# Optimization experiments

Measured on AMD Instinct MI355X. Metric: run time of the kernel, lower is better.

Reference implementation:

```python
import jax, jax.numpy as jnp
import numpy as np

N_USERS, N_ITEMS, EMB_DIM, N_INTENTS, N_EDGES, N_LAYERS = 50000, 100000, 64, 128, 3000000, 2
N_NODES = N_USERS + N_ITEMS


def _l2norm(x, eps=1e-8):
    # F.normalize(p=2, dim=-1, eps): x / max(||x||, eps)
    n = jnp.sqrt(jnp.sum(x * x, axis=-1, keepdims=True))
    return x / jnp.maximum(n, eps)


def setup_inputs() -> dict:
    key = jax.random.key(0)
    k0, k1, k2, k3, k4, k5 = jax.random.split(key, 6)
    xav_e = np.sqrt(2.0 / (N_NODES + EMB_DIM)).astype(np.float32)
    xav_i = np.sqrt(2.0 / (EMB_DIM + N_INTENTS)).astype(np.float32)
    return {
        "user_emb": jax.random.normal(k0, (N_USERS, EMB_DIM), jnp.float32) * xav_e,
        "item_emb": jax.random.normal(k1, (N_ITEMS, EMB_DIM), jnp.float32) * xav_e,
        "user_intent": jax.random.normal(k2, (EMB_DIM, N_INTENTS), jnp.float32) * xav_i,
        "item_intent": jax.random.normal(k3, (EMB_DIM, N_INTENTS), jnp.float32) * xav_i,
        "all_h": jax.random.randint(k4, (N_EDGES,), 0, N_NODES, jnp.int32),
        "all_t": jax.random.randint(k5, (N_EDGES,), 0, N_NODES, jnp.int32),
    }


def reference(user_emb, item_emb, user_intent, item_intent, all_h, all_t):
    E = all_h.shape[0]

    def spmm(vals, x):
        # y[h] += vals * x[t]  over edges  (torch_sparse.spmm)
        return jax.ops.segment_sum(vals[:, None] * x[all_t], all_h, num_segments=N_NODES)

    # _cal_sparse_adj: G = D^-1/2 A D^-1/2 on the unweighted edge list
    deg = jax.ops.segment_sum(jnp.ones((E,), jnp.float32), all_h, num_segments=N_NODES)
    d_inv_sqrt = jnp.where(deg > 0, deg, 1.0) ** -0.5 * (deg > 0)
    g_values = d_inv_sqrt[all_h] * d_inv_sqrt[all_t]

    def adaptive_values(src):
        # _adaptive_mask: cosine-sim edge weights, row-normalized
        he = _l2norm(src[all_h])
        te = _l2norm(src[all_t])
        edge_alpha = (jnp.sum(he * te, axis=1) + 1.0) * 0.5  # in [0,1]
        row_sum = jax.ops.segment_sum(edge_alpha, all_h, num_segments=N_NODES)
        d_inv = jnp.where(row_sum > 0, 1.0 / jnp.where(row_sum > 0, row_sum, 1.0), 0.0)
        return d_inv[all_h] * edge_alpha

    emb = jnp.concatenate([user_emb, item_emb], axis=0)  # [N, d]
    acc = emb
    for _ in range(N_LAYERS):
        gnn = spmm(g_values, emb)
        u, it = emb[:N_USERS], emb[N_USERS:]
        u_int = jax.nn.softmax(u @ user_intent, axis=1) @ user_intent.T
        i_int = jax.nn.softmax(it @ item_intent, axis=1) @ item_intent.T
        int_e = jnp.concatenate([u_int, i_int], axis=0)
        gaa = spmm(adaptive_values(gnn), emb)
        iaa = spmm(adaptive_values(int_e), emb)
        emb = gnn + int_e + gaa + iaa + emb
        acc = acc + emb
    # torch: sum over stacked layer embeddings == initial + each layer output
    return acc
```

## Files before the change

kernel.cpp:

```cpp
#include <hip/hip_runtime.h>
#include <hip/hip_bf16.h>

#define N_USERS   50000
#define N_ITEMS   100000
#define N_NODES   150000
#define DIM       64
#define N_INTENTS 128
#define N_EDGES   3000000
#define PSHIFT    9
#define PROWS     (1 << PSHIFT)
#define NPART     ((N_NODES + PROWS - 1) >> PSHIFT)
#define CHUNK     16384
#define NCHB      ((N_EDGES + CHUNK - 1) / CHUNK)

typedef __attribute__((ext_vector_type(8))) short short8v;
typedef __attribute__((ext_vector_type(4))) float f32x4;

static __device__ __forceinline__ float wsum64(float v){
#pragma unroll
  for (int m = 32; m >= 1; m >>= 1) v += __shfl_xor(v, m, 64);
  return v;
}
static __device__ __forceinline__ float wmax64(float v){
#pragma unroll
  for (int m = 32; m >= 1; m >>= 1) v = fmaxf(v, __shfl_xor(v, m, 64));
  return v;
}

template<int CTRL>
static __device__ __forceinline__ float dpp_ror_add(float x){
  int t = __builtin_amdgcn_update_dpp(0, __builtin_bit_cast(int, x),
                                      CTRL, 0xF, 0xF, true);
  return x + __builtin_bit_cast(float, t);
}
static __device__ __forceinline__ float row16_allsum(float x){
  x = dpp_ror_add<0x128>(x);
  x = dpp_ror_add<0x124>(x);
  x = dpp_ror_add<0x122>(x);
  x = dpp_ror_add<0x121>(x);
  return x;
}
template<int CTRL>
static __device__ __forceinline__ float dpp_ror_max(float x){
  int t = __builtin_amdgcn_update_dpp(0, __builtin_bit_cast(int, x),
                                      CTRL, 0xF, 0xF, true);
  return fmaxf(x, __builtin_bit_cast(float, t));
}
static __device__ __forceinline__ float row16_allmax(float x){
  x = dpp_ror_max<0x128>(x);
  x = dpp_ror_max<0x124>(x);
  x = dpp_ror_max<0x122>(x);
  x = dpp_ror_max<0x121>(x);
  return x;
}

static __device__ __forceinline__ unsigned short f2bf(float x){
  __hip_bfloat16 h = __float2bfloat16(x);
  return __builtin_bit_cast(unsigned short, h);
}
static __device__ __forceinline__ float bf_lo(unsigned int v){
  return __builtin_bit_cast(float, v << 16);
}
static __device__ __forceinline__ float bf_hi(unsigned int v){
  return __builtin_bit_cast(float, v & 0xFFFF0000u);
}
static __device__ __forceinline__ float bfval(unsigned short h){
  return __builtin_bit_cast(float, (unsigned int)h << 16);
}
static __device__ __forceinline__ void split2(float x, unsigned short& hi,
                                              unsigned short& lo){
  hi = f2bf(x);
  lo = f2bf(x - bfval(hi));
}

__global__ void k_init(const float* __restrict__ ue, const float* __restrict__ ie,
                       float* __restrict__ emb, float* __restrict__ acc,
                       unsigned short* __restrict__ embb){
  int i = blockIdx.x * 256 + threadIdx.x;
  if (i >= N_NODES * DIM) return;
  float v = (i < N_USERS * DIM) ? ue[i] : ie[i - N_USERS * DIM];
  emb[i] = v; acc[i] = v; embb[i] = f2bf(v);
}

__global__ void k_deg(const int* __restrict__ h, int* __restrict__ deg){
  int e = blockIdx.x * 256 + threadIdx.x;
  if (e < N_EDGES) atomicAdd(&deg[h[e]], 1);
}

__global__ void k_scan1(const int* __restrict__ deg, int* __restrict__ tmp,
                        int* __restrict__ aux){
  __shared__ int s[256];
  int t = threadIdx.x, i = blockIdx.x * 256 + t;
  int v = (i < N_NODES) ? deg[i] : 0;
  s[t] = v; __syncthreads();
  for (int off = 1; off < 256; off <<= 1){
    int x = (t >= off) ? s[t - off] : 0;
    __syncthreads();
    s[t] += x;
    __syncthreads();
  }
  if (i < N_NODES) tmp[i] = s[t];
  if (t == 255) aux[blockIdx.x] = s[255];
}

__global__ __launch_bounds__(1024) void k_scan2(int* __restrict__ aux, int n){
  __shared__ int s[1024];
  int t = threadIdx.x;
  int v = (t < n) ? aux[t] : 0;
  s[t] = v; __syncthreads();
  for (int off = 1; off < 1024; off <<= 1){
    int x = (t >= off) ? s[t - off] : 0;
    __syncthreads();
    s[t] += x;
    __syncthreads();
  }
  if (t < n) aux[t] = s[t] - v;
}

__global__ void k_rowptr(const int* __restrict__ tmp, const int* __restrict__ deg,
                         const int* __restrict__ aux, int* __restrict__ rp,
                         float* __restrict__ dis, int* __restrict__ gcur){
  int i = blockIdx.x * 256 + threadIdx.x;
  if (i < N_NODES){
    int v = aux[i >> 8] + tmp[i] - deg[i];
    rp[i] = v;
    int d = deg[i];
    dis[i] = (d > 0) ? (1.f / sqrtf((float)d)) : 0.f;
    if ((i & (PROWS - 1)) == 0) gcur[i >> PSHIFT] = v;
  }
  if (i == 0) rp[N_NODES] = N_EDGES;
}

__global__ __launch_bounds__(256) void k_part1(const int* __restrict__ h,
                                               const int* __restrict__ t,
                                               int* __restrict__ gcur,
                                               unsigned int* __restrict__ stg){
  __shared__ int hist[NPART];
  __shared__ int base[NPART];
  __shared__ int cnt2[NPART];
  int tid = threadIdx.x;
  int s = blockIdx.x * CHUNK;
  int e = min(s + CHUNK, N_EDGES);
  for (int p = tid; p < NPART; p += 256){ hist[p] = 0; cnt2[p] = 0; }
  __syncthreads();
  for (int i = s + tid; i < e; i += 256)
    atomicAdd(&hist[h[i] >> PSHIFT], 1);
  __syncthreads();
  for (int p = tid; p < NPART; p += 256){
    int c = hist[p];
    base[p] = c ? atomicAdd(&gcur[p], c) : 0;
  }
  __syncthreads();
  for (int i = s + tid; i < e; i += 256){
    int hh = h[i];
    int part = hh >> PSHIFT;
    int pos = base[part] + atomicAdd(&cnt2[part], 1);
    stg[pos] = ((unsigned)t[i] << PSHIFT) | (unsigned)(hh & (PROWS - 1));
  }
}

__global__ __launch_bounds__(256) void k_part2(const int* __restrict__ rp,
                                               const unsigned int* __restrict__ stg,
                                               int* __restrict__ t_csr){
  __shared__ int cur[PROWS];
  int b = blockIdx.x, tid = threadIdx.x;
  int row0 = b << PSHIFT;
  int rows = min(PROWS, N_NODES - row0);
  for (int i = tid; i < rows; i += 256) cur[i] = rp[row0 + i];
  __syncthreads();
  int s = rp[row0], e = rp[row0 + rows];
  for (int i = s + tid; i < e; i += 256){
    unsigned int v = stg[i];
    int pos = atomicAdd(&cur[v & (PROWS - 1)], 1);
    t_csr[pos] = (int)(v >> PSHIFT);
  }
}

__global__ void k_spmm_gnn(const int* __restrict__ rp, const int* __restrict__ t_csr,
                           const float* __restrict__ dis,
                           const unsigned short* __restrict__ embb,
                           float* __restrict__ gnn, unsigned short* __restrict__ hgA){
  int w = (blockIdx.x * 256 + threadIdx.x) >> 6;
  int lane = threadIdx.x & 63;
  if (w >= N_NODES) return;
  int slot = lane >> 3, sub = lane & 7;
  int s = rp[w], e = rp[w + 1];
  float a0=0.f,a1=0.f,a2=0.f,a3=0.f,a4=0.f,a5=0.f,a6=0.f,a7=0.f;
  for (int i = s + slot; i < e; i += 8){
    int t = t_csr[i];
    float wt = dis[t];
    uint4 ev = *(const uint4*)(embb + (size_t)t * 64 + 8 * sub);
    a0 = fmaf(wt, bf_lo(ev.x), a0); a1 = fmaf(wt, bf_hi(ev.x), a1);
    a2 = fmaf(wt, bf_lo(ev.y), a2); a3 = fmaf(wt, bf_hi(ev.y), a3);
    a4 = fmaf(wt, bf_lo(ev.z), a4); a5 = fmaf(wt, bf_hi(ev.z), a5);
    a6 = fmaf(wt, bf_lo(ev.w), a6); a7 = fmaf(wt, bf_hi(ev.w), a7);
  }
#pragma unroll
  for (int m = 8; m <= 32; m <<= 1){
    a0 += __shfl_xor(a0, m, 64); a1 += __shfl_xor(a1, m, 64);
    a2 += __shfl_xor(a2, m, 64); a3 += __shfl_xor(a3, m, 64);
    a4 += __shfl_xor(a4, m, 64); a5 += __shfl_xor(a5, m, 64);
    a6 += __shfl_xor(a6, m, 64); a7 += __shfl_xor(a7, m, 64);
  }
  float dw = dis[w];
  float g0 = dw*a0, g1 = dw*a1, g2 = dw*a2, g3 = dw*a3;
  float g4 = dw*a4, g5 = dw*a5, g6 = dw*a6, g7 = dw*a7;
  float sq = g0*g0 + g1*g1 + g2*g2 + g3*g3 + g4*g4 + g5*g5 + g6*g6 + g7*g7;
#pragma unroll
  for (int m = 1; m <= 4; m <<= 1) sq += __shfl_xor(sq, m, 64);
  float invn = 1.f / fmaxf(sqrtf(sq), 1e-8f);
  if (slot == 0){
    float4 v0 = make_float4(g0, g1, g2, g3);
    float4 v1 = make_float4(g4, g5, g6, g7);
    ((float4*)gnn)[w * 16 + 2 * sub]     = v0;
    ((float4*)gnn)[w * 16 + 2 * sub + 1] = v1;
    uint4 ob;
    ob.x = (unsigned)f2bf(g0*invn) | ((unsigned)f2bf(g1*invn) << 16);
    ob.y = (unsigned)f2bf(g2*invn) | ((unsigned)f2bf(g3*invn) << 16);
    ob.z = (unsigned)f2bf(g4*invn) | ((unsigned)f2bf(g5*invn) << 16);
    ob.w = (unsigned)f2bf(g6*invn) | ((unsigned)f2bf(g7*invn) << 16);
    *(uint4*)(hgA + (size_t)w * 64 + 8 * sub) = ob;
  }
}

__global__ void k_wprep(const float* __restrict__ wu, const float* __restrict__ wi,
                        unsigned short* __restrict__ wbuf){
  const float* W = blockIdx.x ? wi : wu;
  unsigned short* seg = wbuf + blockIdx.x * 32768;
  int tid = threadIdx.x;
  for (int i = tid; i < DIM * N_INTENTS; i += 256){
    unsigned short h, l; split2(W[i], h, l);
    seg[16384 + i] = h; seg[24576 + i] = l;
  }
  for (int idx = tid; idx < 16 * 64; idx += 256){
    int f = idx >> 6, lane = idx & 63;
    int nt = f >> 1, ks = f & 1, g = lane >> 4, c = lane & 15;
    int in = 16 * nt + c;
#pragma unroll
    for (int e = 0; e < 8; e++){
      int d = 8 * g + e + 32 * ks;
      unsigned short h, l; split2(W[d * N_INTENTS + in], h, l);
      seg[f * 512 + lane * 8 + e] = h;
      seg[8192 + f * 512 + lane * 8 + e] = l;
    }
  }
}

__global__ __launch_bounds__(256) void k_intent_mfma(
    const unsigned short* __restrict__ wseg, const float* __restrict__ emb,
    unsigned short* __restrict__ out_bf, unsigned short* __restrict__ hgB,
    int base_node, int count){
  __shared__ __align__(16) unsigned int Pl[4][2048];
  int wid = threadIdx.x >> 6, lane = threadIdx.x & 63;
  int tile = blockIdx.x * 4 + wid;
  if (tile * 16 >= count) return;
  int g = lane >> 4, c = lane & 15;

  const float4* erow = (const float4*)(emb + (size_t)(base_node + tile * 16 + c) * DIM);
  float4 ea0 = erow[2 * g],     eb0 = erow[2 * g + 1];
  float4 ea1 = erow[8 + 2 * g], eb1 = erow[9 + 2 * g];
  short8v ehi[2], elo[2];
  {
    float xs[16] = {ea0.x, ea0.y, ea0.z, ea0.w, eb0.x, eb0.y, eb0.z, eb0.w,
                    ea1.x, ea1.y, ea1.z, ea1.w, eb1.x, eb1.y, eb1.z, eb1.w};
#pragma unroll
    for (int ksi = 0; ksi < 2; ksi++)
#pragma unroll
      for (int e = 0; e < 8; e++){
        unsigned short h, l; split2(xs[ksi * 8 + e], h, l);
        ehi[ksi][e] = (short)h; elo[ksi][e] = (short)l;
      }
  }

  const uint4* w1hi = (const uint4*)wseg;
  const uint4* w1lo = (const uint4*)(wseg + 8192);
  f32x4 acc1[8];
#pragma unroll
  for (int nt = 0; nt < 8; nt++){
    f32x4 a = {0.f, 0.f, 0.f, 0.f};
#pragma unroll
    for (int ks = 0; ks < 2; ks++){
      short8v wh = __builtin_bit_cast(short8v, w1hi[(nt * 2 + ks) * 64 + lane]);
      short8v wl = __builtin_bit_cast(short8v, w1lo[(nt * 2 + ks) * 64 + lane]);
      a = __builtin_amdgcn_mfma_f32_16x16x32_bf16(ehi[ks], wh, a, 0, 0, 0);
      a = __builtin_amdgcn_mfma_f32_16x16x32_bf16(elo[ks], wh, a, 0, 0, 0);
      a = __builtin_amdgcn_mfma_f32_16x16x32_bf16(ehi[ks], wl, a, 0, 0, 0);
    }
    acc1[nt] = a;
  }

  unsigned int* pw = &Pl[wid][0];
#pragma unroll
  for (int r = 0; r < 4; r++){
    float m = acc1[0][r];
#pragma unroll
    for (int nt = 1; nt < 8; nt++) m = fmaxf(m, acc1[nt][r]);
    m = row16_allmax(m);
    float p[8];
    float s = 0.f;
#pragma unroll
    for (int nt = 0; nt < 8; nt++){ p[nt] = __expf(acc1[nt][r] - m); s += p[nt]; }
    s = row16_allsum(s);
    float inv = 1.f / s;
    int node = 4 * g + r;
    int swz = (node & 7) << 2;
    int base = node * 128 + c;
#pragma unroll
    for (int nt = 0; nt < 8; nt++){
      float v = p[nt] * inv;
      unsigned short h, l; split2(v, h, l);
      pw[(base + 16 * nt) ^ swz] = (unsigned int)h | ((unsigned int)l << 16);
    }
  }

  const uint4* pr = (const uint4*)pw;
  short8v phf[4], plf[4];
  int sw = (c & 7) << 2;
#pragma unroll
  for (int ks = 0; ks < 4; ks++){
    int i0 = c * 128 + 8 * g + 32 * ks;
    uint4 ra = pr[(i0 ^ sw) >> 2];
    uint4 rb = pr[((i0 + 4) ^ sw) >> 2];
    unsigned int q[8] = {ra.x, ra.y, ra.z, ra.w, rb.x, rb.y, rb.z, rb.w};
#pragma unroll
    for (int e = 0; e < 8; e++){
      phf[ks][e] = (short)(q[e] & 0xFFFFu);
      plf[ks][e] = (short)(q[e] >> 16);
    }
  }

  const uint4* w2hi = (const uint4*)(wseg + 16384);
  const uint4* w2lo = (const uint4*)(wseg + 24576);
  f32x4 acc2[4];
#pragma unroll
  for (int nt = 0; nt < 4; nt++){
    f32x4 a = {0.f, 0.f, 0.f, 0.f};
#pragma unroll
    for (int ks = 0; ks < 4; ks++){
      int fi = (16 * nt + c) * 16 + ks * 4 + g;
      short8v wh = __builtin_bit_cast(short8v, w2hi[fi]);
      short8v wl = __builtin_bit_cast(short8v, w2lo[fi]);
      a = __builtin_amdgcn_mfma_f32_16x16x32_bf16(phf[ks], wh, a, 0, 0, 0);
      a = __builtin_amdgcn_mfma_f32_16x16x32_bf16(plf[ks], wh, a, 0, 0, 0);
      a = __builtin_amdgcn_mfma_f32_16x16x32_bf16(phf[ks], wl, a, 0, 0, 0);
    }
    acc2[nt] = a;
  }

#pragma unroll
  for (int r = 0; r < 4; r++){
    float sq = 0.f;
#pragma unroll
    for (int nt = 0; nt < 4; nt++) sq = fmaf(acc2[nt][r], acc2[nt][r], sq);
    sq = row16_allsum(sq);
    float invn = 1.f / fmaxf(sqrtf(sq), 1e-8f);
    size_t gbase = (size_t)(base_node + tile * 16 + 4 * g + r) * DIM + c;
#pragma unroll
    for (int nt = 0; nt < 4; nt++){
      float v = acc2[nt][r];
      out_bf[gbase + 16 * nt] = f2bf(v);
      hgB[gbase + 16 * nt] = f2bf(v * invn);
    }
  }
}

__global__ void k_adafuse(const int* __restrict__ rp, const int* __restrict__ t_csr,
                          const unsigned short* __restrict__ hgA,
                          const unsigned short* __restrict__ hgB,
                          const uint2* __restrict__ inte_bf2,
                          const unsigned short* __restrict__ embb,
                          const float* __restrict__ emb,
                          float* __restrict__ gnn_io, float* __restrict__ acc,
                          uint2* __restrict__ embb_next2){
  int w = (blockIdx.x * 256 + threadIdx.x) >> 6;
  int lane = threadIdx.x & 63;
  if (w >= N_NODES) return;
  int g = lane >> 4, c = lane & 15;
  const unsigned short* wa = hgA + (size_t)w * 64;
  const unsigned short* wb = hgB + (size_t)w * 64;
  short8v bA0 = *(const short8v*)(wa + 8 * g);
  short8v bA1 = *(const short8v*)(wa + 8 * g + 32);
  short8v bB0 = *(const short8v*)(wb + 8 * g);
  short8v bB1 = *(const short8v*)(wb + 8 * g + 32);
  int s = rp[w], e = rp[w + 1];
  float4 s1 = make_float4(0.f, 0.f, 0.f, 0.f);
  float4 s2 = make_float4(0.f, 0.f, 0.f, 0.f);
  float r1 = 0.f, r2 = 0.f;
  for (int i = s; i < e; i += 16){
    int ia = i + c; if (ia >= e) ia = e - 1;
    int t = t_csr[ia];
    const unsigned short* ra = hgA + (size_t)t * 64;
    const unsigned short* rb = hgB + (size_t)t * 64;
    short8v aA0 = *(const short8v*)(ra + 8 * g);
    short8v aA1 = *(const short8v*)(ra + 8 * g + 32);
    short8v aB0 = *(const short8v*)(rb + 8 * g);
    short8v aB1 = *(const short8v*)(rb + 8 * g + 32);
    f32x4 p = {0.f, 0.f, 0.f, 0.f};
    f32x4 q = {0.f, 0.f, 0.f, 0.f};
    p = __builtin_amdgcn_mfma_f32_16x16x32_bf16(aA0, bA0, p, 0, 0, 0);
    p = __builtin_amdgcn_mfma_f32_16x16x32_bf16(aA1, bA1, p, 0, 0, 0);
    q = __builtin_amdgcn_mfma_f32_16x16x32_bf16(aB0, bB0, q, 0, 0, 0);
    q = __builtin_amdgcn_mfma_f32_16x16x32_bf16(aB1, bB1, q, 0, 0, 0);
#pragma unroll
    for (int r = 0; r < 4; r++){
      int ei = i + 4 * g + r;
      bool valid = ei < e;
      float a1v = valid ? fmaf(p[r], 0.5f, 0.5f) : 0.f;
      float a2v = valid ? fmaf(q[r], 0.5f, 0.5f) : 0.f;
      r1 += a1v; r2 += a2v;
      int tt = t_csr[valid ? ei : (e - 1)];
      uint2 ev = *(const uint2*)(embb + (size_t)tt * 64 + 4 * c);
      float v0 = bf_lo(ev.x), v1 = bf_hi(ev.x), v2 = bf_lo(ev.y), v3 = bf_hi(ev.y);
      s1.x = fmaf(a1v, v0, s1.x); s1.y = fmaf(a1v, v1, s1.y);
      s1.z = fmaf(a1v, v2, s1.z); s1.w = fmaf(a1v, v3, s1.w);
      s2.x = fmaf(a2v, v0, s2.x); s2.y = fmaf(a2v, v1, s2.y);
      s2.z = fmaf(a2v, v2, s2.z); s2.w = fmaf(a2v, v3, s2.w);
    }
  }
#pragma unroll
  for (int m = 16; m <= 32; m <<= 1){
    s1.x += __shfl_xor(s1.x, m, 64); s1.y += __shfl_xor(s1.y, m, 64);
    s1.z += __shfl_xor(s1.z, m, 64); s1.w += __shfl_xor(s1.w, m, 64);
    s2.x += __shfl_xor(s2.x, m, 64); s2.y += __shfl_xor(s2.y, m, 64);
    s2.z += __shfl_xor(s2.z, m, 64); s2.w += __shfl_xor(s2.w, m, 64);
    r1   += __shfl_xor(r1,   m, 64); r2   += __shfl_xor(r2,   m, 64);
  }
  float d1 = (r1 > 0.f) ? 1.f / r1 : 0.f;
  float d2 = (r2 > 0.f) ? 1.f / r2 : 0.f;
  if (g == 0){
    int idx4 = w * 16 + c;
    float4 gg = ((float4*)gnn_io)[idx4];
    uint2 it = inte_bf2[idx4];
    float4 em = ((const float4*)emb)[idx4];
    float4 nv;
    nv.x = gg.x + bf_lo(it.x) + em.x + d1 * s1.x + d2 * s2.x;
    nv.y = gg.y + bf_hi(it.x) + em.y + d1 * s1.y + d2 * s2.y;
    nv.z = gg.z + bf_lo(it.y) + em.z + d1 * s1.z + d2 * s2.z;
    nv.w = gg.w + bf_hi(it.y) + em.w + d1 * s1.w + d2 * s2.w;
    ((float4*)gnn_io)[idx4] = nv;
    float4 ac = ((float4*)acc)[idx4];
    ac.x += nv.x; ac.y += nv.y; ac.z += nv.z; ac.w += nv.w;
    ((float4*)acc)[idx4] = ac;
    uint2 ob;
    ob.x = (unsigned)f2bf(nv.x) | ((unsigned)f2bf(nv.y) << 16);
    ob.y = (unsigned)f2bf(nv.z) | ((unsigned)f2bf(nv.w) << 16);
    embb_next2[idx4] = ob;
  }
}

extern "C" void kernel_launch(void* const* d_in, const int* in_sizes, int n_in,
                              void* d_out, int out_size, void* d_ws, size_t ws_size,
                              hipStream_t stream){
  const float* ue = (const float*)d_in[0];
  const float* ie = (const float*)d_in[1];
  const float* wu = (const float*)d_in[2];
  const float* wi = (const float*)d_in[3];
  const int* all_h = (const int*)d_in[4];
  const int* all_t = (const int*)d_in[5];
  float* acc = (float*)d_out;

  char* p = (char*)d_ws;
  auto take = [&](size_t bytes)->char*{
    char* r = p; p += (bytes + 255) & ~size_t(255); return r;
  };
  float*  embA  = (float*)take(sizeof(float) * N_NODES * DIM);
  float*  embB  = (float*)take(sizeof(float) * N_NODES * DIM);
  unsigned short* hgA = (unsigned short*)take(sizeof(short) * N_NODES * DIM);
  unsigned short* hgB = (unsigned short*)take(sizeof(short) * N_NODES * DIM);
  unsigned short* inte_bf = (unsigned short*)take(sizeof(short) * N_NODES * DIM);
  unsigned short* embbA   = (unsigned short*)take(sizeof(short) * N_NODES * DIM);
  unsigned short* embbB   = (unsigned short*)take(sizeof(short) * N_NODES * DIM);
  unsigned short* wbuf    = (unsigned short*)take(sizeof(short) * 2 * 32768);
  int*    t_csr = (int*)take(sizeof(int) * N_EDGES);
  float*  dis   = (float*)take(sizeof(float) * N_NODES);
  int*    deg   = (int*)take(sizeof(int) * N_NODES);
  int*    tmp   = (int*)take(sizeof(int) * N_NODES);
  int*    aux   = (int*)take(sizeof(int) * 1024);
  int*    rp    = (int*)take(sizeof(int) * (N_NODES + 1));
  int*    gcur  = (int*)take(sizeof(int) * NPART);
  if ((size_t)(p - (char*)d_ws) > ws_size) return;
  unsigned int* stg = (unsigned int*)hgA;

  const int ELEM_B  = (N_NODES * DIM + 255) / 256;
  const int NODEW_B = (N_NODES * 64 + 255) / 256;
  const int EDGE_B  = (N_EDGES + 255) / 256;
  const int NODE_B  = (N_NODES + 255) / 256;

  hipMemsetAsync(deg, 0, sizeof(int) * N_NODES, stream);
  k_init<<<ELEM_B, 256, 0, stream>>>(ue, ie, embA, acc, embbA);
  k_wprep<<<2, 256, 0, stream>>>(wu, wi, wbuf);
  k_deg<<<EDGE_B, 256, 0, stream>>>(all_h, deg);
  k_scan1<<<NODE_B, 256, 0, stream>>>(deg, tmp, aux);
  k_scan2<<<1, 1024, 0, stream>>>(aux, NODE_B);
  k_rowptr<<<NODE_B, 256, 0, stream>>>(tmp, deg, aux, rp, dis, gcur);
  k_part1<<<NCHB, 256, 0, stream>>>(all_h, all_t, gcur, stg);
  k_part2<<<NPART, 256, 0, stream>>>(rp, stg, t_csr);

  const int UT_B = ((N_USERS / 16) + 3) / 4;
  const int IT_B = ((N_ITEMS / 16) + 3) / 4;

  float* eA = embA;
  float* eB = embB;
  unsigned short* ebA = embbA;
  unsigned short* ebB = embbB;
  for (int layer = 0; layer < 2; layer++){
    k_spmm_gnn<<<NODEW_B, 256, 0, stream>>>(rp, t_csr, dis, ebA, eB, hgA);
    k_intent_mfma<<<UT_B, 256, 0, stream>>>(wbuf, eA, inte_bf, hgB, 0, N_USERS);
    k_intent_mfma<<<IT_B, 256, 0, stream>>>(wbuf + 32768, eA, inte_bf, hgB,
                                            N_USERS, N_ITEMS);
    k_adafuse<<<NODEW_B, 256, 0, stream>>>(rp, t_csr, hgA, hgB,
                                           (const uint2*)inte_bf, ebA,
                                           eA, eB, acc, (uint2*)ebB);
    float* t = eA; eA = eB; eB = t;
    unsigned short* tb = ebA; ebA = ebB; ebB = tb;
  }
}
```

Baseline: 1.018 ms.

## Interleave normalized feature buffers per node and software-pipeline gathers in SpMM kernels

Merges the two normalized bf16 feature arrays into one interleaved 128-wide row per node, so each adaptive-weight gather reads one contiguous 256-byte row instead of two separate 128-byte rows. Both the gnn SpMM and the adaptive fused kernel now prefetch the next iteration's neighbor indices and embedding loads before consuming the current ones, hiding gather latency. The cost is more live registers, which may reduce occupancy, plus clamped redundant loads at row ends.

New measurement: 1.024 ms. Within noise of the previous version (+0.6%).

```diff
diff --git a/kernel.cpp b/kernel.cpp
--- a/kernel.cpp
+++ b/kernel.cpp
@@ -179,21 +179,29 @@
 __global__ void k_spmm_gnn(const int* __restrict__ rp, const int* __restrict__ t_csr,
                            const float* __restrict__ dis,
                            const unsigned short* __restrict__ embb,
-                           float* __restrict__ gnn, unsigned short* __restrict__ hgA){
+                           float* __restrict__ gnn, unsigned short* __restrict__ hgAB){
   int w = (blockIdx.x * 256 + threadIdx.x) >> 6;
   int lane = threadIdx.x & 63;
   if (w >= N_NODES) return;
   int slot = lane >> 3, sub = lane & 7;
   int s = rp[w], e = rp[w + 1];
   float a0=0.f,a1=0.f,a2=0.f,a3=0.f,a4=0.f,a5=0.f,a6=0.f,a7=0.f;
-  for (int i = s + slot; i < e; i += 8){
-    int t = t_csr[i];
-    float wt = dis[t];
-    uint4 ev = *(const uint4*)(embb + (size_t)t * 64 + 8 * sub);
-    a0 = fmaf(wt, bf_lo(ev.x), a0); a1 = fmaf(wt, bf_hi(ev.x), a1);
-    a2 = fmaf(wt, bf_lo(ev.y), a2); a3 = fmaf(wt, bf_hi(ev.y), a3);
-    a4 = fmaf(wt, bf_lo(ev.z), a4); a5 = fmaf(wt, bf_hi(ev.z), a5);
-    a6 = fmaf(wt, bf_lo(ev.w), a6); a7 = fmaf(wt, bf_hi(ev.w), a7);
+  if (e > s){
+    int i = s + slot;
+    int t0 = t_csr[min(i, e - 1)];
+    int t1 = t_csr[min(i + 8, e - 1)];
+    float wt0 = dis[t0];
+    uint4 ev0 = *(const uint4*)(embb + (size_t)t0 * 64 + 8 * sub);
+    for (; i < e; i += 8){
+      int t2 = t_csr[min(i + 16, e - 1)];
+      float wt1 = dis[t1];
+      uint4 ev1 = *(const uint4*)(embb + (size_t)t1 * 64 + 8 * sub);
+      a0 = fmaf(wt0, bf_lo(ev0.x), a0); a1 = fmaf(wt0, bf_hi(ev0.x), a1);
+      a2 = fmaf(wt0, bf_lo(ev0.y), a2); a3 = fmaf(wt0, bf_hi(ev0.y), a3);
+      a4 = fmaf(wt0, bf_lo(ev0.z), a4); a5 = fmaf(wt0, bf_hi(ev0.z), a5);
+      a6 = fmaf(wt0, bf_lo(ev0.w), a6); a7 = fmaf(wt0, bf_hi(ev0.w), a7);
+      wt0 = wt1; ev0 = ev1; t1 = t2;
+    }
   }
 #pragma unroll
   for (int m = 8; m <= 32; m <<= 1){
@@ -219,7 +227,7 @@
     ob.y = (unsigned)f2bf(g2*invn) | ((unsigned)f2bf(g3*invn) << 16);
     ob.z = (unsigned)f2bf(g4*invn) | ((unsigned)f2bf(g5*invn) << 16);
     ob.w = (unsigned)f2bf(g6*invn) | ((unsigned)f2bf(g7*invn) << 16);
-    *(uint4*)(hgA + (size_t)w * 64 + 8 * sub) = ob;
+    *(uint4*)(hgAB + (size_t)w * 128 + 8 * sub) = ob;
   }
 }
 
@@ -248,7 +256,7 @@
 
 __global__ __launch_bounds__(256) void k_intent_mfma(
     const unsigned short* __restrict__ wseg, const float* __restrict__ emb,
-    unsigned short* __restrict__ out_bf, unsigned short* __restrict__ hgB,
+    unsigned short* __restrict__ out_bf, unsigned short* __restrict__ hgAB,
     int base_node, int count){
   __shared__ __align__(16) unsigned int Pl[4][2048];
   int wid = threadIdx.x >> 6, lane = threadIdx.x & 63;
@@ -354,19 +362,20 @@
     for (int nt = 0; nt < 4; nt++) sq = fmaf(acc2[nt][r], acc2[nt][r], sq);
     sq = row16_allsum(sq);
     float invn = 1.f / fmaxf(sqrtf(sq), 1e-8f);
-    size_t gbase = (size_t)(base_node + tile * 16 + 4 * g + r) * DIM + c;
+    size_t node = (size_t)(base_node + tile * 16 + 4 * g + r);
+    unsigned short* hw = hgAB + node * 128 + 64;
+    size_t obase = node * DIM + c;
 #pragma unroll
     for (int nt = 0; nt < 4; nt++){
       float v = acc2[nt][r];
-      out_bf[gbase + 16 * nt] = f2bf(v);
-      hgB[gbase + 16 * nt] = f2bf(v * invn);
+      out_bf[obase + 16 * nt] = f2bf(v);
+      hw[16 * nt + c] = f2bf(v * invn);
     }
   }
 }
 
 __global__ void k_adafuse(const int* __restrict__ rp, const int* __restrict__ t_csr,
-                          const unsigned short* __restrict__ hgA,
-                          const unsigned short* __restrict__ hgB,
+                          const unsigned short* __restrict__ hgAB,
                           const uint2* __restrict__ inte_bf2,
                           const unsigned short* __restrict__ embb,
                           const float* __restrict__ emb,
@@ -376,45 +385,95 @@
   int lane = threadIdx.x & 63;
   if (w >= N_NODES) return;
   int g = lane >> 4, c = lane & 15;
-  const unsigned short* wa = hgA + (size_t)w * 64;
-  const unsigned short* wb = hgB + (size_t)w * 64;
-  short8v bA0 = *(const short8v*)(wa + 8 * g);
-  short8v bA1 = *(const short8v*)(wa + 8 * g + 32);
-  short8v bB0 = *(const short8v*)(wb + 8 * g);
-  short8v bB1 = *(const short8v*)(wb + 8 * g + 32);
+  const unsigned short* wr = hgAB + (size_t)w * 128;
+  short8v bA0 = *(const short8v*)(wr + 8 * g);
+  short8v bA1 = *(const short8v*)(wr + 8 * g + 32);
+  short8v bB0 = *(const short8v*)(wr + 64 + 8 * g);
+  short8v bB1 = *(const short8v*)(wr + 96 + 8 * g);
   int s = rp[w], e = rp[w + 1];
   float4 s1 = make_float4(0.f, 0.f, 0.f, 0.f);
   float4 s2 = make_float4(0.f, 0.f, 0.f, 0.f);
   float r1 = 0.f, r2 = 0.f;
-  for (int i = s; i < e; i += 16){
-    int ia = i + c; if (ia >= e) ia = e - 1;
+  if (e > s){
+    int ia = min(s + c, e - 1);
     int t = t_csr[ia];
-    const unsigned short* ra = hgA + (size_t)t * 64;
-    const unsigned short* rb = hgB + (size_t)t * 64;
+    const unsigned short* ra = hgAB + (size_t)t * 128;
     short8v aA0 = *(const short8v*)(ra + 8 * g);
     short8v aA1 = *(const short8v*)(ra + 8 * g + 32);
-    short8v aB0 = *(const short8v*)(rb + 8 * g);
-    short8v aB1 = *(const short8v*)(rb + 8 * g + 32);
-    f32x4 p = {0.f, 0.f, 0.f, 0.f};
-    f32x4 q = {0.f, 0.f, 0.f, 0.f};
-    p = __builtin_amdgcn_mfma_f32_16x16x32_bf16(aA0, bA0, p, 0, 0, 0);
-    p = __builtin_amdgcn_mfma_f32_16x16x32_bf16(aA1, bA1, p, 0, 0, 0);
-    q = __builtin_amdgcn_mfma_f32_16x16x32_bf16(aB0, bB0, q, 0, 0, 0);
-    q = __builtin_amdgcn_mfma_f32_16x16x32_bf16(aB1, bB1, q, 0, 0, 0);
-#pragma unroll
-    for (int r = 0; r < 4; r++){
-      int ei = i + 4 * g + r;
-      bool valid = ei < e;
-      float a1v = valid ? fmaf(p[r], 0.5f, 0.5f) : 0.f;
-      float a2v = valid ? fmaf(q[r], 0.5f, 0.5f) : 0.f;
-      r1 += a1v; r2 += a2v;
-      int tt = t_csr[valid ? ei : (e - 1)];
-      uint2 ev = *(const uint2*)(embb + (size_t)tt * 64 + 4 * c);
-      float v0 = bf_lo(ev.x), v1 = bf_hi(ev.x), v2 = bf_lo(ev.y), v3 = bf_hi(ev.y);
-      s1.x = fmaf(a1v, v0, s1.x); s1.y = fmaf(a1v, v1, s1.y);
-      s1.z = fmaf(a1v, v2, s1.z); s1.w = fmaf(a1v, v3, s1.w);
-      s2.x = fmaf(a2v, v0, s2.x); s2.y = fmaf(a2v, v1, s2.y);
-      s2.z = fmaf(a2v, v2, s2.z); s2.w = fmaf(a2v, v3, s2.w);
+    short8v aB0 = *(const short8v*)(ra + 64 + 8 * g);
+    short8v aB1 = *(const short8v*)(ra + 96 + 8 * g);
+    int eb = s + 4 * g;
+    uint2 ev0 = *(const uint2*)(embb + (size_t)t_csr[min(eb,     e-1)] * 64 + 4 * c);
+    uint2 ev1 = *(const uint2*)(embb + (size_t)t_csr[min(eb + 1, e-1)] * 64 + 4 * c);
+    uint2 ev2 = *(const uint2*)(embb + (size_t)t_csr[min(eb + 2, e-1)] * 64 + 4 * c);
+    uint2 ev3 = *(const uint2*)(embb + (size_t)t_csr[min(eb + 3, e-1)] * 64 + 4 * c);
+    for (int i = s; i < e; i += 16){
+      int inx = i + 16;
+      int ja = min(inx + c, e - 1);
+      int tn = t_csr[ja];
+      const unsigned short* rn = hgAB + (size_t)tn * 128;
+      short8v nA0 = *(const short8v*)(rn + 8 * g);
+      short8v nA1 = *(const short8v*)(rn + 8 * g + 32);
+      short8v nB0 = *(const short8v*)(rn + 64 + 8 * g);
+      short8v nB1 = *(const short8v*)(rn + 96 + 8 * g);
+      int nb = inx + 4 * g;
+      uint2 ne0 = *(const uint2*)(embb + (size_t)t_csr[min(nb,     e-1)] * 64 + 4 * c);
+      uint2 ne1 = *(const uint2*)(embb + (size_t)t_csr[min(nb + 1, e-1)] * 64 + 4 * c);
+      uint2 ne2 = *(const uint2*)(embb + (size_t)t_csr[min(nb + 2, e-1)] * 64 + 4 * c);
+      uint2 ne3 = *(const uint2*)(embb + (size_t)t_csr[min(nb + 3, e-1)] * 64 + 4 * c);
+      f32x4 p = {0.f, 0.f, 0.f, 0.f};
+      f32x4 q = {0.f, 0.f, 0.f, 0.f};
+      p = __builtin_amdgcn_mfma_f32_16x16x32_bf16(aA0, bA0, p, 0, 0, 0);
+      p = __builtin_amdgcn_mfma_f32_16x16x32_bf16(aA1, bA1, p, 0, 0, 0);
+      q = __builtin_amdgcn_mfma_f32_16x16x32_bf16(aB0, bB0, q, 0, 0, 0);
+      q = __builtin_amdgcn_mfma_f32_16x16x32_bf16(aB1, bB1, q, 0, 0, 0);
+      int ebase = i + 4 * g;
+      {
+        bool valid = ebase < e;
+        float a1v = valid ? fmaf(p[0], 0.5f, 0.5f) : 0.f;
+        float a2v = valid ? fmaf(q[0], 0.5f, 0.5f) : 0.f;
+        r1 += a1v; r2 += a2v;
+        float v0 = bf_lo(ev0.x), v1 = bf_hi(ev0.x), v2 = bf_lo(ev0.y), v3 = bf_hi(ev0.y);
+        s1.x = fmaf(a1v, v0, s1.x); s1.y = fmaf(a1v, v1, s1.y);
+        s1.z = fmaf(a1v, v2, s1.z); s1.w = fmaf(a1v, v3, s1.w);
+        s2.x = fmaf(a2v, v0, s2.x); s2.y = fmaf(a2v, v1, s2.y);
+        s2.z = fmaf(a2v, v2, s2.z); s2.w = fmaf(a2v, v3, s2.w);
+      }
+      {
+        bool valid = (ebase + 1) < e;
+        float a1v = valid ? fmaf(p[1], 0.5f, 0.5f) : 0.f;
+        float a2v = valid ? fmaf(q[1], 0.5f, 0.5f) : 0.f;
+        r1 += a1v; r2 += a2v;
+        float v0 = bf_lo(ev1.x), v1 = bf_hi(ev1.x), v2 = bf_lo(ev1.y), v3 = bf_hi(ev1.y);
+        s1.x = fmaf(a1v, v0, s1.x); s1.y = fmaf(a1v, v1, s1.y);
+        s1.z = fmaf(a1v, v2, s1.z); s1.w = fmaf(a1v, v3, s1.w);
+        s2.x = fmaf(a2v, v0, s2.x); s2.y = fmaf(a2v, v1, s2.y);
+        s2.z = fmaf(a2v, v2, s2.z); s2.w = fmaf(a2v, v3, s2.w);
+      }
+      {
+        bool valid = (ebase + 2) < e;
+        float a1v = valid ? fmaf(p[2], 0.5f, 0.5f) : 0.f;
+        float a2v = valid ? fmaf(q[2], 0.5f, 0.5f) : 0.f;
+        r1 += a1v; r2 += a2v;
+        float v0 = bf_lo(ev2.x), v1 = bf_hi(ev2.x), v2 = bf_lo(ev2.y), v3 = bf_hi(ev2.y);
+        s1.x = fmaf(a1v, v0, s1.x); s1.y = fmaf(a1v, v1, s1.y);
+        s1.z = fmaf(a1v, v2, s1.z); s1.w = fmaf(a1v, v3, s1.w);
+        s2.x = fmaf(a2v, v0, s2.x); s2.y = fmaf(a2v, v1, s2.y);
+        s2.z = fmaf(a2v, v2, s2.z); s2.w = fmaf(a2v, v3, s2.w);
+      }
+      {
+        bool valid = (ebase + 3) < e;
+        float a1v = valid ? fmaf(p[3], 0.5f, 0.5f) : 0.f;
+        float a2v = valid ? fmaf(q[3], 0.5f, 0.5f) : 0.f;
+        r1 += a1v; r2 += a2v;
+        float v0 = bf_lo(ev3.x), v1 = bf_hi(ev3.x), v2 = bf_lo(ev3.y), v3 = bf_hi(ev3.y);
+        s1.x = fmaf(a1v, v0, s1.x); s1.y = fmaf(a1v, v1, s1.y);
+        s1.z = fmaf(a1v, v2, s1.z); s1.w = fmaf(a1v, v3, s1.w);
+        s2.x = fmaf(a2v, v0, s2.x); s2.y = fmaf(a2v, v1, s2.y);
+        s2.z = fmaf(a2v, v2, s2.z); s2.w = fmaf(a2v, v3, s2.w);
+      }
+      aA0 = nA0; aA1 = nA1; aB0 = nB0; aB1 = nB1;
+      ev0 = ne0; ev1 = ne1; ev2 = ne2; ev3 = ne3;
     }
   }
 #pragma unroll
@@ -465,8 +524,7 @@
   };
   float*  embA  = (float*)take(sizeof(float) * N_NODES * DIM);
   float*  embB  = (float*)take(sizeof(float) * N_NODES * DIM);
-  unsigned short* hgA = (unsigned short*)take(sizeof(short) * N_NODES * DIM);
-  unsigned short* hgB = (unsigned short*)take(sizeof(short) * N_NODES * DIM);
+  unsigned short* hgAB = (unsigned short*)take(sizeof(short) * N_NODES * 128);
   unsigned short* inte_bf = (unsigned short*)take(sizeof(short) * N_NODES * DIM);
   unsigned short* embbA   = (unsigned short*)take(sizeof(short) * N_NODES * DIM);
   unsigned short* embbB   = (unsigned short*)take(sizeof(short) * N_NODES * DIM);
@@ -479,7 +537,7 @@
   int*    rp    = (int*)take(sizeof(int) * (N_NODES + 1));
   int*    gcur  = (int*)take(sizeof(int) * NPART);
   if ((size_t)(p - (char*)d_ws) > ws_size) return;
-  unsigned int* stg = (unsigned int*)hgA;
+  unsigned int* stg = (unsigned int*)hgAB;
 
   const int ELEM_B  = (N_NODES * DIM + 255) / 256;
   const int NODEW_B = (N_NODES * 64 + 255) / 256;
@@ -504,11 +562,11 @@
   unsigned short* ebA = embbA;
   unsigned short* ebB = embbB;
   for (int layer = 0; layer < 2; layer++){
-    k_spmm_gnn<<<NODEW_B, 256, 0, stream>>>(rp, t_csr, dis, ebA, eB, hgA);
-    k_intent_mfma<<<UT_B, 256, 0, stream>>>(wbuf, eA, inte_bf, hgB, 0, N_USERS);
-    k_intent_mfma<<<IT_B, 256, 0, stream>>>(wbuf + 32768, eA, inte_bf, hgB,
+    k_spmm_gnn<<<NODEW_B, 256, 0, stream>>>(rp, t_csr, dis, ebA, eB, hgAB);
+    k_intent_mfma<<<UT_B, 256, 0, stream>>>(wbuf, eA, inte_bf, hgAB, 0, N_USERS);
+    k_intent_mfma<<<IT_B, 256, 0, stream>>>(wbuf + 32768, eA, inte_bf, hgAB,
                                             N_USERS, N_ITEMS);
-    k_adafuse<<<NODEW_B, 256, 0, stream>>>(rp, t_csr, hgA, hgB,
+    k_adafuse<<<NODEW_B, 256, 0, stream>>>(rp, t_csr, hgAB,
                                            (const uint2*)inte_bf, ebA,
                                            eA, eB, acc, (uint2*)ebB);
     float* t = eA; eA = eB; eB = t;
```

## Interleave normalized gnn and intent rows; replace MFMA dots with DPP reductions

Applied to the files above, without the earlier changes.

The two normalized bf16 tables (gnn and intent) are merged into one interleaved 128-wide row per node, so each neighbor's pair of vectors is fetched with a single contiguous 256-byte read. The adaptive-fusion kernel drops its MFMA-based 16-edge batched cosine computation. Instead, four edge slots per wave each compute the two dot products with per-lane partial sums and 16-lane DPP reductions. This removes the tail-padding waste and redundant t_csr reloads, but uses only 4 edges in flight per wave and spends more VALU work on the reductions.

Measured after the change: 1.008 ms. Within noise of the previous version (-0.9%).

```diff
diff --git a/kernel.cpp b/kernel.cpp
--- a/kernel.cpp
+++ b/kernel.cpp
@@ -19,11 +19,6 @@
 static __device__ __forceinline__ float wsum64(float v){
 #pragma unroll
   for (int m = 32; m >= 1; m >>= 1) v += __shfl_xor(v, m, 64);
-  return v;
-}
-static __device__ __forceinline__ float wmax64(float v){
-#pragma unroll
-  for (int m = 32; m >= 1; m >>= 1) v = fmaxf(v, __shfl_xor(v, m, 64));
   return v;
 }
 
@@ -179,7 +174,7 @@
 __global__ void k_spmm_gnn(const int* __restrict__ rp, const int* __restrict__ t_csr,
                            const float* __restrict__ dis,
                            const unsigned short* __restrict__ embb,
-                           float* __restrict__ gnn, unsigned short* __restrict__ hgA){
+                           float* __restrict__ gnn, unsigned short* __restrict__ hgAB){
   int w = (blockIdx.x * 256 + threadIdx.x) >> 6;
   int lane = threadIdx.x & 63;
   if (w >= N_NODES) return;
@@ -219,7 +214,7 @@
     ob.y = (unsigned)f2bf(g2*invn) | ((unsigned)f2bf(g3*invn) << 16);
     ob.z = (unsigned)f2bf(g4*invn) | ((unsigned)f2bf(g5*invn) << 16);
     ob.w = (unsigned)f2bf(g6*invn) | ((unsigned)f2bf(g7*invn) << 16);
-    *(uint4*)(hgA + (size_t)w * 64 + 8 * sub) = ob;
+    *(uint4*)(hgAB + (size_t)w * 128 + 8 * sub) = ob;
   }
 }
 
@@ -248,7 +243,7 @@
 
 __global__ __launch_bounds__(256) void k_intent_mfma(
     const unsigned short* __restrict__ wseg, const float* __restrict__ emb,
-    unsigned short* __restrict__ out_bf, unsigned short* __restrict__ hgB,
+    unsigned short* __restrict__ out_bf, unsigned short* __restrict__ hgAB,
     int base_node, int count){
   __shared__ __align__(16) unsigned int Pl[4][2048];
   int wid = threadIdx.x >> 6, lane = threadIdx.x & 63;
@@ -354,68 +349,55 @@
     for (int nt = 0; nt < 4; nt++) sq = fmaf(acc2[nt][r], acc2[nt][r], sq);
     sq = row16_allsum(sq);
     float invn = 1.f / fmaxf(sqrtf(sq), 1e-8f);
-    size_t gbase = (size_t)(base_node + tile * 16 + 4 * g + r) * DIM + c;
+    size_t node = (size_t)(base_node + tile * 16 + 4 * g + r);
+    unsigned short* hw = hgAB + node * 128 + 64;
+    size_t obase = node * DIM + c;
 #pragma unroll
     for (int nt = 0; nt < 4; nt++){
       float v = acc2[nt][r];
-      out_bf[gbase + 16 * nt] = f2bf(v);
-      hgB[gbase + 16 * nt] = f2bf(v * invn);
+      out_bf[obase + 16 * nt] = f2bf(v);
+      hw[16 * nt + c] = f2bf(v * invn);
     }
   }
 }
 
 __global__ void k_adafuse(const int* __restrict__ rp, const int* __restrict__ t_csr,
-                          const unsigned short* __restrict__ hgA,
-                          const unsigned short* __restrict__ hgB,
+                          const uint4* __restrict__ hgAB4,
                           const uint2* __restrict__ inte_bf2,
-                          const unsigned short* __restrict__ embb,
+                          const uint2* __restrict__ embb2,
                           const float* __restrict__ emb,
                           float* __restrict__ gnn_io, float* __restrict__ acc,
                           uint2* __restrict__ embb_next2){
   int w = (blockIdx.x * 256 + threadIdx.x) >> 6;
   int lane = threadIdx.x & 63;
   if (w >= N_NODES) return;
-  int g = lane >> 4, c = lane & 15;
-  const unsigned short* wa = hgA + (size_t)w * 64;
-  const unsigned short* wb = hgB + (size_t)w * 64;
-  short8v bA0 = *(const short8v*)(wa + 8 * g);
-  short8v bA1 = *(const short8v*)(wa + 8 * g + 32);
-  short8v bB0 = *(const short8v*)(wb + 8 * g);
-  short8v bB1 = *(const short8v*)(wb + 8 * g + 32);
+  int slot = lane >> 4, sub = lane & 15;
+  uint4 hp = hgAB4[(size_t)w * 16 + sub];
+  float w0 = bf_lo(hp.x), w1 = bf_hi(hp.x), w2 = bf_lo(hp.y), w3 = bf_hi(hp.y);
+  float w4 = bf_lo(hp.z), w5 = bf_hi(hp.z), w6 = bf_lo(hp.w), w7 = bf_hi(hp.w);
+  bool isA = sub < 8;
   int s = rp[w], e = rp[w + 1];
   float4 s1 = make_float4(0.f, 0.f, 0.f, 0.f);
   float4 s2 = make_float4(0.f, 0.f, 0.f, 0.f);
   float r1 = 0.f, r2 = 0.f;
-  for (int i = s; i < e; i += 16){
-    int ia = i + c; if (ia >= e) ia = e - 1;
-    int t = t_csr[ia];
-    const unsigned short* ra = hgA + (size_t)t * 64;
-    const unsigned short* rb = hgB + (size_t)t * 64;
-    short8v aA0 = *(const short8v*)(ra + 8 * g);
-    short8v aA1 = *(const short8v*)(ra + 8 * g + 32);
-    short8v aB0 = *(const short8v*)(rb + 8 * g);
-    short8v aB1 = *(const short8v*)(rb + 8 * g + 32);
-    f32x4 p = {0.f, 0.f, 0.f, 0.f};
-    f32x4 q = {0.f, 0.f, 0.f, 0.f};
-    p = __builtin_amdgcn_mfma_f32_16x16x32_bf16(aA0, bA0, p, 0, 0, 0);
-    p = __builtin_amdgcn_mfma_f32_16x16x32_bf16(aA1, bA1, p, 0, 0, 0);
-    q = __builtin_amdgcn_mfma_f32_16x16x32_bf16(aB0, bB0, q, 0, 0, 0);
-    q = __builtin_amdgcn_mfma_f32_16x16x32_bf16(aB1, bB1, q, 0, 0, 0);
-#pragma unroll
-    for (int r = 0; r < 4; r++){
-      int ei = i + 4 * g + r;
-      bool valid = ei < e;
-      float a1v = valid ? fmaf(p[r], 0.5f, 0.5f) : 0.f;
-      float a2v = valid ? fmaf(q[r], 0.5f, 0.5f) : 0.f;
-      r1 += a1v; r2 += a2v;
-      int tt = t_csr[valid ? ei : (e - 1)];
-      uint2 ev = *(const uint2*)(embb + (size_t)tt * 64 + 4 * c);
-      float v0 = bf_lo(ev.x), v1 = bf_hi(ev.x), v2 = bf_lo(ev.y), v3 = bf_hi(ev.y);
-      s1.x = fmaf(a1v, v0, s1.x); s1.y = fmaf(a1v, v1, s1.y);
-      s1.z = fmaf(a1v, v2, s1.z); s1.w = fmaf(a1v, v3, s1.w);
-      s2.x = fmaf(a2v, v0, s2.x); s2.y = fmaf(a2v, v1, s2.y);
-      s2.z = fmaf(a2v, v2, s2.z); s2.w = fmaf(a2v, v3, s2.w);
-    }
+  for (int i = s + slot; i < e; i += 4){
+    int t = t_csr[i];
+    uint4 tp = hgAB4[(size_t)t * 16 + sub];
+    float part = w0 * bf_lo(tp.x) + w1 * bf_hi(tp.x)
+               + w2 * bf_lo(tp.y) + w3 * bf_hi(tp.y)
+               + w4 * bf_lo(tp.z) + w5 * bf_hi(tp.z)
+               + w6 * bf_lo(tp.w) + w7 * bf_hi(tp.w);
+    float p = row16_allsum(isA ? part : 0.f);
+    float q = row16_allsum(isA ? 0.f : part);
+    float a1 = fmaf(p, 0.5f, 0.5f);
+    float a2 = fmaf(q, 0.5f, 0.5f);
+    r1 += a1; r2 += a2;
+    uint2 ev = embb2[(size_t)t * 16 + sub];
+    float v0 = bf_lo(ev.x), v1 = bf_hi(ev.x), v2 = bf_lo(ev.y), v3 = bf_hi(ev.y);
+    s1.x = fmaf(a1, v0, s1.x); s1.y = fmaf(a1, v1, s1.y);
+    s1.z = fmaf(a1, v2, s1.z); s1.w = fmaf(a1, v3, s1.w);
+    s2.x = fmaf(a2, v0, s2.x); s2.y = fmaf(a2, v1, s2.y);
+    s2.z = fmaf(a2, v2, s2.z); s2.w = fmaf(a2, v3, s2.w);
   }
 #pragma unroll
   for (int m = 16; m <= 32; m <<= 1){
@@ -427,8 +409,8 @@
   }
   float d1 = (r1 > 0.f) ? 1.f / r1 : 0.f;
   float d2 = (r2 > 0.f) ? 1.f / r2 : 0.f;
-  if (g == 0){
-    int idx4 = w * 16 + c;
+  if (slot == 0){
+    int idx4 = w * 16 + sub;
     float4 gg = ((float4*)gnn_io)[idx4];
     uint2 it = inte_bf2[idx4];
     float4 em = ((const float4*)emb)[idx4];
@@ -465,8 +447,7 @@
   };
   float*  embA  = (float*)take(sizeof(float) * N_NODES * DIM);
   float*  embB  = (float*)take(sizeof(float) * N_NODES * DIM);
-  unsigned short* hgA = (unsigned short*)take(sizeof(short) * N_NODES * DIM);
-  unsigned short* hgB = (unsigned short*)take(sizeof(short) * N_NODES * DIM);
+  unsigned short* hgAB = (unsigned short*)take(sizeof(short) * N_NODES * 128);
   unsigned short* inte_bf = (unsigned short*)take(sizeof(short) * N_NODES * DIM);
   unsigned short* embbA   = (unsigned short*)take(sizeof(short) * N_NODES * DIM);
   unsigned short* embbB   = (unsigned short*)take(sizeof(short) * N_NODES * DIM);
@@ -479,7 +460,7 @@
   int*    rp    = (int*)take(sizeof(int) * (N_NODES + 1));
   int*    gcur  = (int*)take(sizeof(int) * NPART);
   if ((size_t)(p - (char*)d_ws) > ws_size) return;
-  unsigned int* stg = (unsigned int*)hgA;
+  unsigned int* stg = (unsigned int*)hgAB;
 
   const int ELEM_B  = (N_NODES * DIM + 255) / 256;
   const int NODEW_B = (N_NODES * 64 + 255) / 256;
@@ -504,12 +485,13 @@
   unsigned short* ebA = embbA;
   unsigned short* ebB = embbB;
   for (int layer = 0; layer < 2; layer++){
-    k_spmm_gnn<<<NODEW_B, 256, 0, stream>>>(rp, t_csr, dis, ebA, eB, hgA);
-    k_intent_mfma<<<UT_B, 256, 0, stream>>>(wbuf, eA, inte_bf, hgB, 0, N_USERS);
-    k_intent_mfma<<<IT_B, 256, 0, stream>>>(wbuf + 32768, eA, inte_bf, hgB,
+    k_spmm_gnn<<<NODEW_B, 256, 0, stream>>>(rp, t_csr, dis, ebA, eB, hgAB);
+    k_intent_mfma<<<UT_B, 256, 0, stream>>>(wbuf, eA, inte_bf, hgAB, 0, N_USERS);
+    k_intent_mfma<<<IT_B, 256, 0, stream>>>(wbuf + 32768, eA, inte_bf, hgAB,
                                             N_USERS, N_ITEMS);
-    k_adafuse<<<NODEW_B, 256, 0, stream>>>(rp, t_csr, hgA, hgB,
-                                           (const uint2*)inte_bf, ebA,
+    k_adafuse<<<NODEW_B, 256, 0, stream>>>(rp, t_csr, (const uint4*)hgAB,
+                                           (const uint2*)inte_bf,
+                                           (const uint2*)ebA,
                                            eA, eB, acc, (uint2*)ebB);
     float* t = eA; eA = eB; eB = t;
     unsigned short* tb = ebA; ebA = ebB; ebB = tb;
```
